# Performance work log

Measured on AMD Instinct MI355X. Metric: run time of the kernel, lower is better.

## Reference

```python
import jax, jax.numpy as jnp
import numpy as np

N_NODES = 50000
N_EDGES = 800000
IN_FEATS = 128
OUT_CLASSES = 128


def _glorot(key, shape):
    fan_in, fan_out = shape[1], shape[0]
    limit = float(np.sqrt(6.0 / (fan_in + fan_out)))
    return jax.random.uniform(key, shape, jnp.float32, -limit, limit)


def setup_inputs() -> dict:
    key = jax.random.key(0)
    ks = jax.random.split(key, 11)
    x = jax.random.normal(ks[0], (N_NODES, IN_FEATS), jnp.float32)
    edge_index = jax.random.randint(ks[1], (2, N_EDGES), 0, N_NODES, jnp.int64)
    h = OUT_CLASSES // 2
    # PyG SAGEConv: lin_l applied to aggregated neighbors (has bias), lin_r to root (no bias)
    return {
        "x": x,
        "edge_index": edge_index,
        "W_l1": _glorot(ks[2], (OUT_CLASSES, IN_FEATS)),
        "b1": jnp.zeros((OUT_CLASSES,), jnp.float32),
        "W_r1": _glorot(ks[3], (OUT_CLASSES, IN_FEATS)),
        "W_l2": _glorot(ks[4], (h, OUT_CLASSES)),
        "b2": jnp.zeros((h,), jnp.float32),
        "W_r2": _glorot(ks[5], (h, OUT_CLASSES)),
        "W_l3": _glorot(ks[6], (OUT_CLASSES, h)),
        "b3": jnp.zeros((OUT_CLASSES,), jnp.float32),
        "W_r3": _glorot(ks[7], (OUT_CLASSES, h)),
    }


def _sage_conv(x, src, dst, W_l, b, W_r):
    # gather source-node features, mean-aggregate at destinations
    msgs = x[src]                                               # [E, d]
    agg = jax.ops.segment_sum(msgs, dst, num_segments=N_NODES)  # [N, d]
    cnt = jax.ops.segment_sum(jnp.ones((src.shape[0], 1), x.dtype), dst,
                              num_segments=N_NODES)             # [N, 1]
    mean = agg / jnp.maximum(cnt, 1.0)
    return mean @ W_l.T + b + x @ W_r.T


def reference(x, edge_index, W_l1, b1, W_r1, W_l2, b2, W_r2, W_l3, b3, W_r3):
    src, dst = edge_index[0], edge_index[1]
    h = _sage_conv(x, src, dst, W_l1, b1, W_r1)
    h = _sage_conv(h, src, dst, W_l2, b2, W_r2)
    h = _sage_conv(h, src, dst, W_l3, b3, W_r3)
    return h
```

## Files before the change

kernel.cpp:

```cpp
#include <hip/hip_runtime.h>

#define N_NODES 50000
#define N_EDGES 800000
#define BUCKETS 196
#define ECHUNK 4096
#define EBLKS 196
#define BCAP 5120

typedef __attribute__((ext_vector_type(8))) _Float16 half8;
typedef __attribute__((ext_vector_type(4))) float f32x4;


__global__ __launch_bounds__(256) void prep_k(
    const int* __restrict__ src, const int* __restrict__ dst,
    int* __restrict__ gcur, unsigned* __restrict__ binned,
    const float* __restrict__ x, _Float16* __restrict__ xh,
    const float* __restrict__ Wl1, const float* __restrict__ Wr1,
    const float* __restrict__ Wl2, const float* __restrict__ Wr2,
    const float* __restrict__ Wl3, const float* __restrict__ Wr3,
    _Float16* ph_l1, _Float16* pl_l1, _Float16* ph_r1, _Float16* pl_r1,
    _Float16* ph_c2, _Float16* pl_c2, _Float16* ph_l3, _Float16* pl_l3,
    _Float16* ph_r3, _Float16* pl_r3) {
  int blk = blockIdx.x;
  int t = threadIdx.x;
  if (blk < EBLKS) {
    __shared__ int h[BUCKETS];
    __shared__ int base[BUCKETS];
    for (int i = t; i < BUCKETS; i += 256) h[i] = 0;
    __syncthreads();
    int e0 = blk * ECHUNK;
    int eend = e0 + ECHUNK < N_EDGES ? e0 + ECHUNK : N_EDGES;
    for (int e = e0 + t; e < eend; e += 256) atomicAdd(&h[dst[e] >> 8], 1);
    __syncthreads();
    for (int i = t; i < BUCKETS; i += 256) {
      if (h[i]) base[i] = atomicAdd(&gcur[i], h[i]);
      h[i] = 0;
    }
    __syncthreads();
    for (int e = e0 + t; e < eend; e += 256) {
      int d = dst[e];
      int b = d >> 8;
      int r = atomicAdd(&h[b], 1);
      binned[(size_t)b * BCAP + base[b] + r] =
          (unsigned)src[e] | ((unsigned)(d & 255) << 16);
    }
  } else if (blk < EBLKS + 32) {
    int g = (blk - EBLKS) * 256 + t;
    const float *S0, *S1 = nullptr;
    _Float16 *ph, *pl;
    int f, K;
    if (g < 2048)      { f = g;        ph = ph_l1; pl = pl_l1; S0 = Wl1; K = 128; }
    else if (g < 4096) { f = g - 2048; ph = ph_r1; pl = pl_r1; S0 = Wr1; K = 128; }
    else if (g < 6144) { f = g - 4096; ph = ph_c2; pl = pl_c2; S0 = Wl2; S1 = Wr2; K = 128; }
    else if (g < 7168) { f = g - 6144; ph = ph_l3; pl = pl_l3; S0 = Wl3; K = 64; }
    else               { f = g - 7168; ph = ph_r3; pl = pl_r3; S0 = Wr3; K = 64; }
    int kb = f >> 9;
    int rem = f & 511;
    int n = rem >> 2;
    int lq = rem & 3;
    const float* srow =
        (S1 && n >= 64) ? (S1 + (size_t)(n - 64) * K) : (S0 + (size_t)n * K);
    int kbase = kb * 32 + lq * 8;
#pragma unroll
    for (int j = 0; j < 8; ++j) {
      float v = srow[kbase + j];
      _Float16 hi = (_Float16)v;
      ph[f * 8 + j] = hi;
      pl[f * 8 + j] = (_Float16)(v - (float)hi);
    }
  } else {
    int i = (blk - EBLKS - 32) * 256 + t;
    if (i >= N_NODES * 16) return;
    const float4* xp = (const float4*)x;
    float4 a = xp[2 * i];
    float4 b = xp[2 * i + 1];
    half8 hh;
    hh[0] = (_Float16)a.x; hh[1] = (_Float16)a.y; hh[2] = (_Float16)a.z; hh[3] = (_Float16)a.w;
    hh[4] = (_Float16)b.x; hh[5] = (_Float16)b.y; hh[6] = (_Float16)b.z; hh[7] = (_Float16)b.w;
    ((half8*)xh)[i] = hh;
  }
}

__global__ __launch_bounds__(256) void bucket_fill_k(const unsigned* __restrict__ binned,
                                                     const int* __restrict__ gcnt,
                                                     int* __restrict__ offs,
                                                     int* __restrict__ deg,
                                                     unsigned short* __restrict__ csr) {
  __shared__ int cnt[256];
  __shared__ int loc[256];
  __shared__ int cur[256];
  int b = blockIdx.x;
  int t = threadIdx.x;
  int base = b * BCAP;
  int end = base + gcnt[b];
  cnt[t] = 0;
  __syncthreads();
  for (int e = base + t; e < end; e += 256) atomicAdd(&cnt[(binned[e] >> 16) & 255], 1);
  __syncthreads();
  loc[t] = cnt[t];
  __syncthreads();
  for (int o = 1; o < 256; o <<= 1) {
    int v = (t >= o) ? loc[t - o] : 0;
    __syncthreads();
    loc[t] += v;
    __syncthreads();
  }
  int excl = loc[t] - cnt[t];
  int node = b * 256 + t;
  if (node < N_NODES) {
    offs[node] = base + excl;
    deg[node] = cnt[t];
  }
  cur[t] = excl;
  __syncthreads();
  for (int e = base + t; e < end; e += 256) {
    unsigned r = binned[e];
    int dl = (r >> 16) & 255;
    int p = atomicAdd(&cur[dl], 1);
    csr[base + p] = (unsigned short)(r & 0xFFFF);
  }
}


template <int D, bool FUSE>
__global__ __launch_bounds__(256) void agg_f16_k(const _Float16* __restrict__ in,
                                                 _Float16* __restrict__ out,
                                                 const int* __restrict__ offs,
                                                 const int* __restrict__ deg,
                                                 const unsigned short* __restrict__ csr,
                                                 const float* __restrict__ bias,
                                                 const _Float16* __restrict__ addend) {
  constexpr int L = D / 8;
  constexpr int NPB = 256 / L;
  int node = blockIdx.x * NPB + threadIdx.x / L;
  int lane = threadIdx.x & (L - 1);
  if (node >= N_NODES) return;
  int start = offs[node];
  int d = deg[node];
  const half8* ip = (const half8*)in;
  float acc[8];
#pragma unroll
  for (int j = 0; j < 8; ++j) acc[j] = 0.f;
  int e = 0;
  for (; e + 8 <= d; e += 8) {
    int s[8];
#pragma unroll
    for (int j = 0; j < 8; ++j) s[j] = csr[start + e + j];
    half8 v[8];
#pragma unroll
    for (int j = 0; j < 8; ++j) v[j] = ip[(size_t)s[j] * L + lane];
#pragma unroll
    for (int j = 0; j < 8; ++j)
#pragma unroll
      for (int q = 0; q < 8; ++q) acc[q] += (float)v[j][q];
  }
  for (; e + 4 <= d; e += 4) {
    int s[4];
#pragma unroll
    for (int j = 0; j < 4; ++j) s[j] = csr[start + e + j];
    half8 v[4];
#pragma unroll
    for (int j = 0; j < 4; ++j) v[j] = ip[(size_t)s[j] * L + lane];
#pragma unroll
    for (int j = 0; j < 4; ++j)
#pragma unroll
      for (int q = 0; q < 8; ++q) acc[q] += (float)v[j][q];
  }
  for (; e < d; ++e) {
    half8 v0 = ip[(size_t)csr[start + e] * L + lane];
#pragma unroll
    for (int q = 0; q < 8; ++q) acc[q] += (float)v0[q];
  }
  float inv = d > 0 ? 1.0f / (float)d : 0.0f;
  half8 o;
  if constexpr (FUSE) {
    half8 av = ((const half8*)addend)[(size_t)node * L + lane];
#pragma unroll
    for (int q = 0; q < 8; ++q)
      o[q] = (_Float16)(acc[q] * inv + bias[lane * 8 + q] + (float)av[q]);
  } else {
#pragma unroll
    for (int q = 0; q < 8; ++q) o[q] = (_Float16)(acc[q] * inv);
  }
  ((half8*)out)[(size_t)node * L + lane] = o;
}


template <int K, bool OUT32>
__global__ __launch_bounds__(256, 4) void fused_agg_gemm_k(
    const _Float16* __restrict__ feat,
    const int* __restrict__ offs, const int* __restrict__ deg,
    const unsigned short* __restrict__ csr,
    const _Float16* __restrict__ Wlh, const _Float16* __restrict__ Wll,
    const _Float16* __restrict__ Wrh, const _Float16* __restrict__ Wrl,
    const float* __restrict__ bias, _Float16* __restrict__ C16,
    float* __restrict__ C32) {
  constexpr int L = K / 8;
  constexpr int CONC = 256 / L;
  constexpr int ITER = 64 / CONC;
  constexpr int STRIDE = K + 8;
  constexpr int KB = K / 32;
  __shared__ _Float16 Asm[64 * STRIDE];
  int t = threadIdx.x;
  int base = blockIdx.x * 64;
  const half8* ip = (const half8*)feat;
  {
    int lane = t & (L - 1);
    int slot = t / L;
#pragma unroll
    for (int it = 0; it < ITER; ++it) {
      int r = it * CONC + slot;
      int node = base + r;
      float acc[8];
#pragma unroll
      for (int j = 0; j < 8; ++j) acc[j] = 0.f;
      float inv = 0.f;
      if (node < N_NODES) {
        int start = offs[node];
        int d = deg[node];
        int e = 0;
        for (; e + 8 <= d; e += 8) {
          int s[8];
#pragma unroll
          for (int j = 0; j < 8; ++j) s[j] = csr[start + e + j];
          half8 v[8];
#pragma unroll
          for (int j = 0; j < 8; ++j) v[j] = ip[(size_t)s[j] * L + lane];
#pragma unroll
          for (int j = 0; j < 8; ++j)
#pragma unroll
            for (int q = 0; q < 8; ++q) acc[q] += (float)v[j][q];
        }
        for (; e + 4 <= d; e += 4) {
          int s[4];
#pragma unroll
          for (int j = 0; j < 4; ++j) s[j] = csr[start + e + j];
          half8 v[4];
#pragma unroll
          for (int j = 0; j < 4; ++j) v[j] = ip[(size_t)s[j] * L + lane];
#pragma unroll
          for (int j = 0; j < 4; ++j)
#pragma unroll
            for (int q = 0; q < 8; ++q) acc[q] += (float)v[j][q];
        }
        for (; e < d; ++e) {
          half8 v0 = ip[(size_t)csr[start + e] * L + lane];
#pragma unroll
          for (int q = 0; q < 8; ++q) acc[q] += (float)v0[q];
        }
        inv = d > 0 ? 1.0f / (float)d : 0.0f;
      }
      half8 o;
#pragma unroll
      for (int q = 0; q < 8; ++q) o[q] = (_Float16)(acc[q] * inv);
      *(half8*)&Asm[r * STRIDE + lane * 8] = o;
    }
  }
  __syncthreads();
  int wave = t >> 6;
  int lane = t & 63;
  int l15 = lane & 15;
  int lq = lane >> 4;
  int row0 = base + wave * 16;
  const int woff = (l15 * 4 + lq) * 8;
  f32x4 acc[8];
#pragma unroll
  for (int c = 0; c < 8; ++c) acc[c] = (f32x4){0.f, 0.f, 0.f, 0.f};
  {
    const _Float16* asrc = &Asm[(wave * 16 + l15) * STRIDE + lq * 8];
    half8 af[KB];
#pragma unroll
    for (int kb = 0; kb < KB; ++kb) af[kb] = *(const half8*)(asrc + kb * 32);
#pragma unroll
    for (int kb = 0; kb < KB; ++kb) {
#pragma unroll
      for (int ct = 0; ct < 8; ++ct) {
        size_t bi = (size_t)(kb * 128 + ct * 16) * 32 + woff;
        half8 bh = *(const half8*)(Wlh + bi);
        half8 bl = *(const half8*)(Wll + bi);
        acc[ct] = __builtin_amdgcn_mfma_f32_16x16x32_f16(af[kb], bh, acc[ct], 0, 0, 0);
        acc[ct] = __builtin_amdgcn_mfma_f32_16x16x32_f16(af[kb], bl, acc[ct], 0, 0, 0);
      }
    }
  }
  {
    int arow = row0 + l15;
    if (arow >= N_NODES) arow = N_NODES - 1;
    const _Float16* ab = feat + (size_t)arow * K + lq * 8;
    half8 af[KB];
#pragma unroll
    for (int kb = 0; kb < KB; ++kb) af[kb] = *(const half8*)(ab + kb * 32);
#pragma unroll
    for (int kb = 0; kb < KB; ++kb) {
#pragma unroll
      for (int ct = 0; ct < 8; ++ct) {
        size_t bi = (size_t)(kb * 128 + ct * 16) * 32 + woff;
        half8 bh = *(const half8*)(Wrh + bi);
        half8 bl = *(const half8*)(Wrl + bi);
        acc[ct] = __builtin_amdgcn_mfma_f32_16x16x32_f16(af[kb], bh, acc[ct], 0, 0, 0);
        acc[ct] = __builtin_amdgcn_mfma_f32_16x16x32_f16(af[kb], bl, acc[ct], 0, 0, 0);
      }
    }
  }
#pragma unroll
  for (int r = 0; r < 4; ++r) {
    int row = row0 + lq * 4 + r;
    if (row >= N_NODES) continue;
#pragma unroll
    for (int ct = 0; ct < 8; ++ct) {
      int col = ct * 16 + l15;
      float v = acc[ct][r] + bias[col];
      if constexpr (OUT32)
        C32[(size_t)row * 128 + col] = v;
      else
        C16[(size_t)row * 128 + col] = (_Float16)v;
    }
  }
}


template <int K, bool DUAL, bool SPLIT, bool OUT32>
__global__ __launch_bounds__(256, 2) void gemm_f16_k(
    const _Float16* __restrict__ A1, const _Float16* __restrict__ W1h,
    const _Float16* __restrict__ W1l,
    const _Float16* __restrict__ A2, const _Float16* __restrict__ W2h,
    const _Float16* __restrict__ W2l,
    const float* __restrict__ bias, _Float16* __restrict__ C16,
    float* __restrict__ C32, _Float16* __restrict__ O2) {
  int wave = threadIdx.x >> 6;
  int lane = threadIdx.x & 63;
  int l15 = lane & 15;
  int lq = lane >> 4;
  int rowblk = blockIdx.x >> 1;
  int colg = blockIdx.x & 1;
  int rg = rowblk * 4 + wave;
  if (rg >= N_NODES / 16) return;
  int row0 = rg << 4;
  constexpr int KB = K / 32;
  constexpr int NN = 128;
  const int woff = (l15 * 4 + lq) * 8;
  f32x4 acc[4];
#pragma unroll
  for (int c = 0; c < 4; ++c) acc[c] = (f32x4){0.f, 0.f, 0.f, 0.f};
  constexpr int NOP = DUAL ? 2 : 1;
#pragma unroll
  for (int op = 0; op < NOP; ++op) {
    const _Float16* A = op ? A2 : A1;
    const _Float16* Wh = op ? W2h : W1h;
    const _Float16* Wl = op ? W2l : W1l;
    const _Float16* ab = A + (size_t)(row0 + l15) * K + lq * 8;
    half8 af[KB];
#pragma unroll
    for (int kb = 0; kb < KB; ++kb) af[kb] = *(const half8*)(ab + kb * 32);
#pragma unroll
    for (int kb = 0; kb < KB; ++kb) {
#pragma unroll
      for (int ct = 0; ct < 4; ++ct) {
        int n0 = colg * 64 + ct * 16;
        size_t base = (size_t)(kb * NN + n0) * 32 + woff;
        half8 bh = *(const half8*)(Wh + base);
        half8 bl = *(const half8*)(Wl + base);
        acc[ct] = __builtin_amdgcn_mfma_f32_16x16x32_f16(af[kb], bh, acc[ct], 0, 0, 0);
        acc[ct] = __builtin_amdgcn_mfma_f32_16x16x32_f16(af[kb], bl, acc[ct], 0, 0, 0);
      }
    }
  }
#pragma unroll
  for (int r = 0; r < 4; ++r) {
    int row = row0 + lq * 4 + r;
#pragma unroll
    for (int ct = 0; ct < 4; ++ct) {
      int col = colg * 64 + ct * 16 + l15;
      float v = acc[ct][r];
      if constexpr (SPLIT) {
        if (col < 64)
          C16[(size_t)row * 64 + col] = (_Float16)v;
        else
          O2[(size_t)row * 64 + (col - 64)] = (_Float16)v;
      } else {
        v += bias[col];
        if constexpr (OUT32)
          C32[(size_t)row * 128 + col] = v;
        else
          C16[(size_t)row * 128 + col] = (_Float16)v;
      }
    }
  }
}

extern "C" void kernel_launch(void* const* d_in, const int* in_sizes, int n_in,
                              void* d_out, int out_size, void* d_ws, size_t ws_size,
                              hipStream_t stream) {
  const float* x   = (const float*)d_in[0];
  const int* ei    = (const int*)d_in[1];
  const float* Wl1 = (const float*)d_in[2];
  const float* b1  = (const float*)d_in[3];
  const float* Wr1 = (const float*)d_in[4];
  const float* Wl2 = (const float*)d_in[5];
  const float* b2  = (const float*)d_in[6];
  const float* Wr2 = (const float*)d_in[7];
  const float* Wl3 = (const float*)d_in[8];
  const float* b3  = (const float*)d_in[9];
  const float* Wr3 = (const float*)d_in[10];
  float* out = (float*)d_out;

  const int* src = ei;
  const int* dst = ei + N_EDGES;

  char* ws = (char*)d_ws;
  size_t off = 0;
  auto take = [&](size_t bytes) {
    void* p = ws + off;
    off += (bytes + 255) & ~(size_t)255;
    return p;
  };
  int* deg    = (int*)take((size_t)N_NODES * 4);
  int* offs   = (int*)take((size_t)N_NODES * 4);
  int* gcur   = (int*)take((size_t)BUCKETS * 4);
  unsigned* binned = (unsigned*)take((size_t)BUCKETS * BCAP * 4);
  unsigned short* csr = (unsigned short*)take((size_t)BUCKETS * BCAP * 2);
  _Float16* xh  = (_Float16*)take((size_t)N_NODES * 128 * 2);
  _Float16* h1h = (_Float16*)take((size_t)N_NODES * 128 * 2);
  _Float16* Ph  = (_Float16*)take((size_t)N_NODES * 64 * 2);
  _Float16* Rh  = (_Float16*)take((size_t)N_NODES * 64 * 2);
  _Float16* h2h = (_Float16*)take((size_t)N_NODES * 64 * 2);
  _Float16* ph_l1 = (_Float16*)take(16384 * 2);
  _Float16* pl_l1 = (_Float16*)take(16384 * 2);
  _Float16* ph_r1 = (_Float16*)take(16384 * 2);
  _Float16* pl_r1 = (_Float16*)take(16384 * 2);
  _Float16* ph_c2 = (_Float16*)take(16384 * 2);
  _Float16* pl_c2 = (_Float16*)take(16384 * 2);
  _Float16* ph_l3 = (_Float16*)take(8192 * 2);
  _Float16* pl_l3 = (_Float16*)take(8192 * 2);
  _Float16* ph_r3 = (_Float16*)take(8192 * 2);
  _Float16* pl_r3 = (_Float16*)take(8192 * 2);

  hipMemsetAsync(gcur, 0, (size_t)BUCKETS * 4, stream);

  prep_k<<<EBLKS + 32 + 3125, 256, 0, stream>>>(
      src, dst, gcur, binned, x, xh, Wl1, Wr1, Wl2, Wr2, Wl3, Wr3, ph_l1, pl_l1,
      ph_r1, pl_r1, ph_c2, pl_c2, ph_l3, pl_l3, ph_r3, pl_r3);
  bucket_fill_k<<<BUCKETS, 256, 0, stream>>>(binned, gcur, offs, deg, csr);

  fused_agg_gemm_k<128, false><<<782, 256, 0, stream>>>(
      xh, offs, deg, csr, ph_l1, pl_l1, ph_r1, pl_r1, b1, h1h, nullptr);

  gemm_f16_k<128, false, true, false><<<1564, 256, 0, stream>>>(
      h1h, ph_c2, pl_c2, nullptr, nullptr, nullptr, nullptr, Ph, nullptr, Rh);
  agg_f16_k<64, true><<<1563, 256, 0, stream>>>(Ph, h2h, offs, deg, csr, b2, Rh);

  fused_agg_gemm_k<64, true><<<782, 256, 0, stream>>>(
      h2h, offs, deg, csr, ph_l3, pl_l3, ph_r3, pl_r3, b3, nullptr, out);
}
```

Baseline: 255.5 us.

## Shrink fused agg-GEMM tiles to one node per lane-group and split columns across waves

```diff
diff --git a/kernel.cpp b/kernel.cpp
--- a/kernel.cpp
+++ b/kernel.cpp
@@ -186,8 +186,8 @@
 }
 
 
-template <int K, bool OUT32>
-__global__ __launch_bounds__(256, 4) void fused_agg_gemm_k(
+template <int K, int NB, bool OUT32>
+__global__ __launch_bounds__(256, 8) void fused_agg_gemm_k(
     const _Float16* __restrict__ feat,
     const int* __restrict__ offs, const int* __restrict__ deg,
     const unsigned short* __restrict__ csr,
@@ -196,86 +196,86 @@
     const float* __restrict__ bias, _Float16* __restrict__ C16,
     float* __restrict__ C32) {
   constexpr int L = K / 8;
-  constexpr int CONC = 256 / L;
-  constexpr int ITER = 64 / CONC;
+  static_assert(256 / L == NB, "one lane-group per node");
   constexpr int STRIDE = K + 8;
   constexpr int KB = K / 32;
-  __shared__ _Float16 Asm[64 * STRIDE];
+  constexpr int ROWG = NB / 16;
+  constexpr int WPR = 4 / ROWG;
+  constexpr int CT = 8 / WPR;
+  __shared__ _Float16 Asm[NB * STRIDE];
   int t = threadIdx.x;
-  int base = blockIdx.x * 64;
+  int base = blockIdx.x * NB;
   const half8* ip = (const half8*)feat;
   {
     int lane = t & (L - 1);
     int slot = t / L;
-#pragma unroll
-    for (int it = 0; it < ITER; ++it) {
-      int r = it * CONC + slot;
-      int node = base + r;
-      float acc[8];
-#pragma unroll
-      for (int j = 0; j < 8; ++j) acc[j] = 0.f;
-      float inv = 0.f;
-      if (node < N_NODES) {
-        int start = offs[node];
-        int d = deg[node];
-        int e = 0;
-        for (; e + 8 <= d; e += 8) {
-          int s[8];
-#pragma unroll
-          for (int j = 0; j < 8; ++j) s[j] = csr[start + e + j];
-          half8 v[8];
-#pragma unroll
-          for (int j = 0; j < 8; ++j) v[j] = ip[(size_t)s[j] * L + lane];
-#pragma unroll
-          for (int j = 0; j < 8; ++j)
-#pragma unroll
-            for (int q = 0; q < 8; ++q) acc[q] += (float)v[j][q];
-        }
-        for (; e + 4 <= d; e += 4) {
-          int s[4];
-#pragma unroll
-          for (int j = 0; j < 4; ++j) s[j] = csr[start + e + j];
-          half8 v[4];
-#pragma unroll
-          for (int j = 0; j < 4; ++j) v[j] = ip[(size_t)s[j] * L + lane];
-#pragma unroll
-          for (int j = 0; j < 4; ++j)
-#pragma unroll
-            for (int q = 0; q < 8; ++q) acc[q] += (float)v[j][q];
-        }
-        for (; e < d; ++e) {
-          half8 v0 = ip[(size_t)csr[start + e] * L + lane];
-#pragma unroll
-          for (int q = 0; q < 8; ++q) acc[q] += (float)v0[q];
-        }
-        inv = d > 0 ? 1.0f / (float)d : 0.0f;
-      }
-      half8 o;
-#pragma unroll
-      for (int q = 0; q < 8; ++q) o[q] = (_Float16)(acc[q] * inv);
-      *(half8*)&Asm[r * STRIDE + lane * 8] = o;
-    }
+    int node = base + slot;
+    float acc[8];
+#pragma unroll
+    for (int j = 0; j < 8; ++j) acc[j] = 0.f;
+    float inv = 0.f;
+    if (node < N_NODES) {
+      int start = offs[node];
+      int d = deg[node];
+      int e = 0;
+      for (; e + 8 <= d; e += 8) {
+        int s[8];
+#pragma unroll
+        for (int j = 0; j < 8; ++j) s[j] = csr[start + e + j];
+        half8 v[8];
+#pragma unroll
+        for (int j = 0; j < 8; ++j) v[j] = ip[(size_t)s[j] * L + lane];
+#pragma unroll
+        for (int j = 0; j < 8; ++j)
+#pragma unroll
+          for (int q = 0; q < 8; ++q) acc[q] += (float)v[j][q];
+      }
+      for (; e + 4 <= d; e += 4) {
+        int s[4];
+#pragma unroll
+        for (int j = 0; j < 4; ++j) s[j] = csr[start + e + j];
+        half8 v[4];
+#pragma unroll
+        for (int j = 0; j < 4; ++j) v[j] = ip[(size_t)s[j] * L + lane];
+#pragma unroll
+        for (int j = 0; j < 4; ++j)
+#pragma unroll
+          for (int q = 0; q < 8; ++q) acc[q] += (float)v[j][q];
+      }
+      for (; e < d; ++e) {
+        half8 v0 = ip[(size_t)csr[start + e] * L + lane];
+#pragma unroll
+        for (int q = 0; q < 8; ++q) acc[q] += (float)v0[q];
+      }
+      inv = d > 0 ? 1.0f / (float)d : 0.0f;
+    }
+    half8 o;
+#pragma unroll
+    for (int q = 0; q < 8; ++q) o[q] = (_Float16)(acc[q] * inv);
+    *(half8*)&Asm[slot * STRIDE + lane * 8] = o;
   }
   __syncthreads();
   int wave = t >> 6;
   int lane = t & 63;
   int l15 = lane & 15;
   int lq = lane >> 4;
-  int row0 = base + wave * 16;
+  int rowg = wave / WPR;
+  int colbase = (wave % WPR) * (CT * 16);
+  int row0 = base + rowg * 16;
   const int woff = (l15 * 4 + lq) * 8;
-  f32x4 acc[8];
-#pragma unroll
-  for (int c = 0; c < 8; ++c) acc[c] = (f32x4){0.f, 0.f, 0.f, 0.f};
+  f32x4 acc[CT];
+#pragma unroll
+  for (int c = 0; c < CT; ++c) acc[c] = (f32x4){0.f, 0.f, 0.f, 0.f};
   {
-    const _Float16* asrc = &Asm[(wave * 16 + l15) * STRIDE + lq * 8];
+    const _Float16* asrc = &Asm[(rowg * 16 + l15) * STRIDE + lq * 8];
     half8 af[KB];
 #pragma unroll
     for (int kb = 0; kb < KB; ++kb) af[kb] = *(const half8*)(asrc + kb * 32);
 #pragma unroll
     for (int kb = 0; kb < KB; ++kb) {
 #pragma unroll
-      for (int ct = 0; ct < 8; ++ct) {
-        size_t bi = (size_t)(kb * 128 + ct * 16) * 32 + woff;
+      for (int ct = 0; ct < CT; ++ct) {
+        size_t bi = (size_t)(kb * 128 + colbase + ct * 16) * 32 + woff;
         half8 bh = *(const half8*)(Wlh + bi);
         half8 bl = *(const half8*)(Wll + bi);
         acc[ct] = __builtin_amdgcn_mfma_f32_16x16x32_f16(af[kb], bh, acc[ct], 0, 0, 0);
@@ -293,8 +293,8 @@
 #pragma unroll
     for (int kb = 0; kb < KB; ++kb) {
 #pragma unroll
-      for (int ct = 0; ct < 8; ++ct) {
-        size_t bi = (size_t)(kb * 128 + ct * 16) * 32 + woff;
+      for (int ct = 0; ct < CT; ++ct) {
+        size_t bi = (size_t)(kb * 128 + colbase + ct * 16) * 32 + woff;
         half8 bh = *(const half8*)(Wrh + bi);
         half8 bl = *(const half8*)(Wrl + bi);
         acc[ct] = __builtin_amdgcn_mfma_f32_16x16x32_f16(af[kb], bh, acc[ct], 0, 0, 0);
@@ -307,8 +307,8 @@
     int row = row0 + lq * 4 + r;
     if (row >= N_NODES) continue;
 #pragma unroll
-    for (int ct = 0; ct < 8; ++ct) {
-      int col = ct * 16 + l15;
+    for (int ct = 0; ct < CT; ++ct) {
+      int col = colbase + ct * 16 + l15;
       float v = acc[ct][r] + bias[col];
       if constexpr (OUT32)
         C32[(size_t)row * 128 + col] = v;
@@ -442,13 +442,13 @@
       ph_r1, pl_r1, ph_c2, pl_c2, ph_l3, pl_l3, ph_r3, pl_r3);
   bucket_fill_k<<<BUCKETS, 256, 0, stream>>>(binned, gcur, offs, deg, csr);
 
-  fused_agg_gemm_k<128, false><<<782, 256, 0, stream>>>(
+  fused_agg_gemm_k<128, 16, false><<<3125, 256, 0, stream>>>(
       xh, offs, deg, csr, ph_l1, pl_l1, ph_r1, pl_r1, b1, h1h, nullptr);
 
   gemm_f16_k<128, false, true, false><<<1564, 256, 0, stream>>>(
       h1h, ph_c2, pl_c2, nullptr, nullptr, nullptr, nullptr, Ph, nullptr, Rh);
   agg_f16_k<64, true><<<1563, 256, 0, stream>>>(Ph, h2h, offs, deg, csr, b2, Rh);
 
-  fused_agg_gemm_k<64, true><<<782, 256, 0, stream>>>(
+  fused_agg_gemm_k<64, 32, true><<<1563, 256, 0, stream>>>(
       h2h, offs, deg, csr, ph_l3, pl_l3, ph_r3, pl_r3, b3, nullptr, out);
 }
```

Measured after the change: 275.1 us. 7.7% more time.
